# Optimization experiments

Measured on AMD Instinct MI355X. Metric: run time of the kernel, lower is better.

Reference implementation:

```python
import jax, jax.numpy as jnp
import numpy as np

N = 65536          # nodes
E = 1048576        # edges
IN_C = 128
HID_C = 32
HEADS = 4
OUT_C = 64
NEG_SLOPE = 0.2
EPS = 1e-16


def gat_conv(x, edge_index, W, att_src, att_dst, bias, heads, out_c, concat):
    """PyG-style GATConv. x: [N, F_in]; edge_index: [2, E] (row=src, col=dst).
    W: [F_in, heads*out_c]; att_src/att_dst: [heads, out_c]; bias: [heads*out_c] or [out_c]."""
    src, dst = edge_index[0], edge_index[1]
    n = x.shape[0]
    h = (x @ W).reshape(n, heads, out_c)                      # [N, H, C]
    a_src = jnp.einsum('nhc,hc->nh', h, att_src)              # [N, H]
    a_dst = jnp.einsum('nhc,hc->nh', h, att_dst)              # [N, H]
    alpha = a_src[src] + a_dst[dst]                           # [E, H]
    alpha = jax.nn.leaky_relu(alpha, NEG_SLOPE)
    # segment softmax over incoming edges of each destination node
    amax = jax.ops.segment_max(alpha, dst, num_segments=n)    # [N, H]
    alpha = jnp.exp(alpha - amax[dst])
    denom = jax.ops.segment_sum(alpha, dst, num_segments=n)   # [N, H]
    alpha = alpha / (denom[dst] + EPS)
    # weighted scatter-add aggregation
    msgs = alpha[:, :, None] * h[src]                         # [E, H, C]
    out = jax.ops.segment_sum(msgs, dst, num_segments=n)      # [N, H, C]
    if concat:
        out = out.reshape(n, heads * out_c)
    else:
        out = out.mean(axis=1)
    return out + bias


def setup_inputs() -> dict:
    key = jax.random.key(0)
    ks = jax.random.split(key, 10)
    s_in = 1.0 / np.sqrt(IN_C)
    s_h = 1.0 / np.sqrt(HEADS * HID_C)
    x = jax.random.normal(ks[0], (N, IN_C), dtype=jnp.float32)
    edge_index = jax.random.randint(ks[1], (2, E), 0, N, dtype=jnp.int64)
    W1 = jax.random.normal(ks[2], (IN_C, HEADS * HID_C), dtype=jnp.float32) * s_in
    att_src1 = jax.random.normal(ks[3], (HEADS, HID_C), dtype=jnp.float32) * s_h
    att_dst1 = jax.random.normal(ks[4], (HEADS, HID_C), dtype=jnp.float32) * s_h
    b1 = jnp.zeros((HEADS * HID_C,), dtype=jnp.float32)
    W2 = jax.random.normal(ks[5], (HEADS * HID_C, OUT_C), dtype=jnp.float32) * s_h
    att_src2 = jax.random.normal(ks[6], (1, OUT_C), dtype=jnp.float32) * s_h
    att_dst2 = jax.random.normal(ks[7], (1, OUT_C), dtype=jnp.float32) * s_h
    b2 = jnp.zeros((OUT_C,), dtype=jnp.float32)
    return {"x": x, "edge_index": edge_index, "W1": W1, "att_src1": att_src1,
            "att_dst1": att_dst1, "b1": b1, "W2": W2, "att_src2": att_src2,
            "att_dst2": att_dst2, "b2": b2}


def reference(x, edge_index, W1, att_src1, att_dst1, b1, W2, att_src2, att_dst2, b2):
    # dropout is identity in eval mode
    h = gat_conv(x, edge_index, W1, att_src1, att_dst1, b1, HEADS, HID_C, concat=True)
    h = jax.nn.sigmoid(h)
    h = gat_conv(h, edge_index, W2, att_src2, att_dst2, b2, 1, OUT_C, concat=True)
    return jax.nn.sigmoid(h)
```

## Files before the change

kernel.cpp:

```cpp
#include <hip/hip_runtime.h>
#include <hip/hip_fp16.h>

#define N_NODES 65536
#define N_EDGES 1048576
#define NBUCK 256
#define PBLOCKS 1024
#define EPB (N_EDGES / PBLOCKS)
#define K4CAP 6144
#define GB1 (N_NODES / 64)
constexpr float NEG = 0.2f;
constexpr float EPS_ = 1e-16f;
constexpr float WSHIFT = 2.7725887f;

typedef __attribute__((ext_vector_type(8))) short bf16x8;
typedef __attribute__((ext_vector_type(4))) float f32x4;

__device__ __forceinline__ unsigned short f2bf(float f) {
    unsigned int u = __float_as_uint(f);
    return (unsigned short)((u + 0x7fffu + ((u >> 16) & 1u)) >> 16);
}
__device__ __forceinline__ unsigned short f2h(float f) {
    __half_raw r = __half_raw(__float2half(f));
    return r.x;
}
__device__ __forceinline__ __half2 u2h2(unsigned int u) {
    union { unsigned int u; __half2 h; } c; c.u = u; return c.h;
}
__device__ __forceinline__ unsigned int h22u(__half2 h) {
    union { unsigned int u; __half2 h; } c; c.h = h; return c.u;
}
__device__ __forceinline__ float lrelu_exp_s(float l) {
    return __expf(fmaxf(l, NEG * l) - WSHIFT);
}


__global__ __launch_bounds__(1024) void scan_a(const int* __restrict__ in,
                                               int* __restrict__ out,
                                               int* __restrict__ bsum) {
    __shared__ int sm[1024];
    int t = threadIdx.x, i = blockIdx.x * 1024 + t;
    int v = in[i];
    sm[t] = v;
    __syncthreads();
    for (int off = 1; off < 1024; off <<= 1) {
        int u = (t >= off) ? sm[t - off] : 0;
        __syncthreads();
        sm[t] += u;
        __syncthreads();
    }
    out[i] = sm[t] - v;
    if (t == 1023) bsum[blockIdx.x] = sm[t];
}

__global__ __launch_bounds__(256) void partition_kernel(const int* __restrict__ ei,
                                                        const int* __restrict__ cursor_mat,
                                                        const int* __restrict__ bsum,
                                                        unsigned int* __restrict__ edge_part) {
    __shared__ int h[NBUCK];
    __shared__ int start[NBUCK];
    __shared__ int cur[NBUCK];
    __shared__ int gcur[NBUCK];
    __shared__ int bs[NBUCK];
    __shared__ unsigned int stage[EPB];
    int t = threadIdx.x;
    h[t] = 0;
    int bsv = bsum[t];
    bs[t] = bsv;
    __syncthreads();
    unsigned int ent[EPB / 256];
    int base = blockIdx.x * EPB;
    #pragma unroll
    for (int i = 0; i < EPB / 256; ++i) {
        int e = base + i * 256 + t;
        int s = ei[e], d = ei[N_EDGES + e];
        ent[i] = ((unsigned int)s << 16) | (unsigned int)d;
        atomicAdd(&h[d >> 8], 1);
    }
    __syncthreads();
    int v = h[t];
    start[t] = v;
    __syncthreads();
    for (int off = 1; off < 256; off <<= 1) {
        int u1 = (t >= off) ? start[t - off] : 0;
        int u2 = (t >= off) ? bs[t - off] : 0;
        __syncthreads();
        start[t] += u1;
        bs[t] += u2;
        __syncthreads();
    }
    int excl = start[t] - v;
    start[t] = excl;
    cur[t] = excl;
    gcur[t] = cursor_mat[t * PBLOCKS + blockIdx.x] + (bs[t] - bsv);
    __syncthreads();
    #pragma unroll
    for (int i = 0; i < EPB / 256; ++i) {
        int b = (int)((ent[i] & 0xffffu) >> 8);
        int slot = atomicAdd(&cur[b], 1);
        stage[slot] = ent[i];
    }
    __syncthreads();
    int s0 = t * (EPB / 256);
    #pragma unroll
    for (int i = 0; i < EPB / 256; ++i) {
        unsigned int p = stage[s0 + i];
        int b = (int)((p & 0xffffu) >> 8);
        edge_part[gcur[b] + (s0 + i - start[b])] = p;
    }
}

__global__ __launch_bounds__(1024) void finalize_kernel(const unsigned int* __restrict__ edge_part,
                                                        const int* __restrict__ cursor_mat,
                                                        const int* __restrict__ bsum,
                                                        int* __restrict__ row_ptr,
                                                        unsigned short* __restrict__ csr16) {
    __shared__ int h[256];
    __shared__ int sc[256];
    __shared__ int cur[256];
    __shared__ int bs[256];
    __shared__ unsigned short stage[K4CAP];
    int t = threadIdx.x;
    int b = blockIdx.x;
    if (b == NBUCK - 1 && t == 0) row_ptr[N_NODES] = N_EDGES;
    if (t < 256) bs[t] = bsum[t];
    __syncthreads();
    for (int off = 1; off < 256; off <<= 1) {
        int u = (t < 256 && t >= off) ? bs[t - off] : 0;
        __syncthreads();
        if (t < 256) bs[t] += u;
        __syncthreads();
    }
    int cs = cursor_mat[b * PBLOCKS] + (b ? bs[b - 1] : 0);
    int ce = (b == NBUCK - 1) ? N_EDGES : cursor_mat[(b + 1) * PBLOCKS] + bs[b];
    int cnt = ce - cs;
    if (t < 256) h[t] = 0;
    __syncthreads();
    for (int i = t; i < cnt; i += 1024)
        atomicAdd(&h[edge_part[cs + i] & 0xffu], 1);
    __syncthreads();
    int v = 0;
    if (t < 256) { v = h[t]; sc[t] = v; }
    __syncthreads();
    for (int off = 1; off < 256; off <<= 1) {
        int u = (t < 256 && t >= off) ? sc[t - off] : 0;
        __syncthreads();
        if (t < 256) sc[t] += u;
        __syncthreads();
    }
    if (t < 256) {
        int excl = sc[t] - v;
        row_ptr[b * 256 + t] = cs + excl;
        cur[t] = excl;
    }
    __syncthreads();
    if (cnt <= K4CAP) {
        for (int i = t; i < cnt; i += 1024) {
            unsigned int p = edge_part[cs + i];
            int slot = atomicAdd(&cur[p & 0xffu], 1);
            stage[slot] = (unsigned short)(p >> 16);
        }
        __syncthreads();
        for (int i = t; i < cnt; i += 1024)
            csr16[cs + i] = stage[i];
    } else {
        for (int i = t; i < cnt; i += 1024) {
            unsigned int p = edge_part[cs + i];
            int slot = atomicAdd(&cur[p & 0xffu], 1);
            csr16[cs + slot] = (unsigned short)(p >> 16);
        }
    }
}


__global__ __launch_bounds__(256) void gemm1_hist(const float* __restrict__ X,
                                                  const float* __restrict__ W,
                                                  const float* __restrict__ as_w,
                                                  const float* __restrict__ ad_w,
                                                  const int* __restrict__ ei,
                                                  unsigned short* __restrict__ H,
                                                  float* __restrict__ a_src,
                                                  float* __restrict__ a_dst,
                                                  int* __restrict__ hist_mat) {
    extern __shared__ unsigned short Wl[];
    int t = threadIdx.x;
    if (blockIdx.x >= GB1) {
        int* hs = (int*)Wl;
        int pb = blockIdx.x - GB1;
        hs[t] = 0;
        __syncthreads();
        int base = pb * EPB;
        #pragma unroll
        for (int i = 0; i < EPB / 256; ++i) {
            int d = ei[N_EDGES + base + i * 256 + t];
            atomicAdd(&hs[d >> 8], 1);
        }
        __syncthreads();
        hist_mat[t * PBLOCKS + pb] = hs[t];
        return;
    }
    constexpr int OUTC = 128;
    constexpr int NT = OUTC / 16;
    for (int idx = t; idx < OUTC * 128; idx += 256) {
        int j = idx & 7;
        int ln = (idx >> 3) & 63;
        int fc = idx >> 9;
        int kc = fc & 3, ct = fc >> 2;
        int k = kc * 32 + (ln >> 4) * 8 + j;
        int nn = ct * 16 + (ln & 15);
        Wl[idx] = (unsigned short)f2bf(W[k * OUTC + nn]);
    }
    __syncthreads();
    int wave = t >> 6, lane = t & 63;
    int m = lane & 15, quad = lane >> 4;
    int node_base = blockIdx.x * 64 + wave * 16;
    const float* xrow = X + (size_t)(node_base + m) * 128 + quad * 8;
    bf16x8 a[4];
    #pragma unroll
    for (int kc = 0; kc < 4; ++kc) {
        float4 u = *(const float4*)(xrow + kc * 32);
        float4 v = *(const float4*)(xrow + kc * 32 + 4);
        bf16x8 af;
        af[0] = (short)f2bf(u.x); af[1] = (short)f2bf(u.y);
        af[2] = (short)f2bf(u.z); af[3] = (short)f2bf(u.w);
        af[4] = (short)f2bf(v.x); af[5] = (short)f2bf(v.y);
        af[6] = (short)f2bf(v.z); af[7] = (short)f2bf(v.w);
        a[kc] = af;
    }
    float asv[NT], adv[NT];
    #pragma unroll
    for (int ct = 0; ct < NT; ++ct) {
        asv[ct] = as_w[ct * 16 + m];
        adv[ct] = ad_w[ct * 16 + m];
    }
    float ps[4][4] = {};
    float pd[4][4] = {};
    #pragma unroll
    for (int ct = 0; ct < NT; ++ct) {
        f32x4 acc = {0.f, 0.f, 0.f, 0.f};
        #pragma unroll
        for (int kc = 0; kc < 4; ++kc) {
            bf16x8 bfr = *(const bf16x8*)(Wl + ((ct * 4 + kc) * 64 + lane) * 8);
            acc = __builtin_amdgcn_mfma_f32_16x16x32_bf16(a[kc], bfr, acc, 0, 0, 0);
        }
        int hh = ct >> 1;
        #pragma unroll
        for (int r = 0; r < 4; ++r) {
            H[(size_t)(node_base + quad * 4 + r) * OUTC + ct * 16 + m] = f2h(acc[r]);
            ps[r][hh] += acc[r] * asv[ct];
            pd[r][hh] += acc[r] * adv[ct];
        }
    }
    #pragma unroll
    for (int r = 0; r < 4; ++r) {
        #pragma unroll
        for (int hh = 0; hh < 4; ++hh) {
            float s = ps[r][hh], d = pd[r][hh];
            #pragma unroll
            for (int msk = 1; msk < 16; msk <<= 1) {
                s += __shfl_xor(s, msk);
                d += __shfl_xor(d, msk);
            }
            if (m == 0) {
                int node = node_base + quad * 4 + r;
                a_src[node * 4 + hh] = s;
                a_dst[node * 4 + hh] = d;
            }
        }
    }
}


__global__ __launch_bounds__(256) void gemm2_mfma(const unsigned short* __restrict__ X,
                                                  const float* __restrict__ W,
                                                  const float* __restrict__ as_w,
                                                  const float* __restrict__ ad_w,
                                                  unsigned short* __restrict__ H,
                                                  float* __restrict__ a_src,
                                                  float* __restrict__ a_dst) {
    constexpr int OUTC = 64;
    constexpr int NT = OUTC / 16;
    extern __shared__ unsigned short Wl[];
    int t = threadIdx.x;
    for (int idx = t; idx < OUTC * 128; idx += 256) {
        int j = idx & 7;
        int ln = (idx >> 3) & 63;
        int fc = idx >> 9;
        int kc = fc & 3, ct = fc >> 2;
        int k = kc * 32 + (ln >> 4) * 8 + j;
        int nn = ct * 16 + (ln & 15);
        Wl[idx] = (unsigned short)f2bf(W[k * OUTC + nn]);
    }
    __syncthreads();
    int wave = t >> 6, lane = t & 63;
    int m = lane & 15, quad = lane >> 4;
    int node_base = blockIdx.x * 64 + wave * 16;
    const unsigned short* xrow = X + (size_t)(node_base + m) * 128 + quad * 8;
    bf16x8 a[4];
    #pragma unroll
    for (int kc = 0; kc < 4; ++kc) a[kc] = *(const bf16x8*)(xrow + kc * 32);
    float asv[NT], adv[NT];
    #pragma unroll
    for (int ct = 0; ct < NT; ++ct) {
        asv[ct] = as_w[ct * 16 + m];
        adv[ct] = ad_w[ct * 16 + m];
    }
    float ps[4] = {};
    float pd[4] = {};
    #pragma unroll
    for (int ct = 0; ct < NT; ++ct) {
        f32x4 acc = {0.f, 0.f, 0.f, 0.f};
        #pragma unroll
        for (int kc = 0; kc < 4; ++kc) {
            bf16x8 bfr = *(const bf16x8*)(Wl + ((ct * 4 + kc) * 64 + lane) * 8);
            acc = __builtin_amdgcn_mfma_f32_16x16x32_bf16(a[kc], bfr, acc, 0, 0, 0);
        }
        #pragma unroll
        for (int r = 0; r < 4; ++r) {
            H[(size_t)(node_base + quad * 4 + r) * OUTC + ct * 16 + m] = f2h(acc[r]);
            ps[r] += acc[r] * asv[ct];
            pd[r] += acc[r] * adv[ct];
        }
    }
    #pragma unroll
    for (int r = 0; r < 4; ++r) {
        float s = ps[r], d = pd[r];
        #pragma unroll
        for (int msk = 1; msk < 16; msk <<= 1) {
            s += __shfl_xor(s, msk);
            d += __shfl_xor(d, msk);
        }
        if (m == 0) {
            int node = node_base + quad * 4 + r;
            a_src[node] = s;
            a_dst[node] = d;
        }
    }
}


__global__ __launch_bounds__(256) void agg1_kernel(const int* __restrict__ row_ptr,
                                                   const unsigned short* __restrict__ csr16,
                                                   const unsigned int* __restrict__ h1u,
                                                   const float* __restrict__ a_src,
                                                   const float* __restrict__ a_dst,
                                                   const float* __restrict__ b1,
                                                   unsigned short* __restrict__ x2) {
    int wave = (blockIdx.x * 256 + threadIdx.x) >> 6;
    int lane = threadIdx.x & 63;
    int half = lane >> 5;
    int ln = lane & 31;
    int n = wave * 2 + half;
    int j8 = ln & 7;
    int whead = ln >> 3;
    int sub = ln >> 4;
    int col = ln & 15;
    int hd_c = col >> 2;
    int rbase = half * 32 + hd_c * 8 + sub;
    float adw = a_dst[n * 4 + whead];
    const unsigned int* h1c = h1u + col * 4;
    const float* asw = a_src + whead;
    int e = row_ptr[n], end = row_ptr[n + 1];
    __half2 acc0 = u2h2(0u), acc1 = u2h2(0u), acc2 = u2h2(0u), acc3 = u2h2(0u);
    float denom = 0.f;
    while (e < end) {
        int rem = end - e;
        int mbA = rem > 8 ? 8 : rem;
        int remB = rem - 8;
        int mbB = remB > 8 ? 8 : (remB > 0 ? remB : 0);
        int idxA = e + (j8 < mbA ? j8 : 0);
        int idxB = (remB > 0) ? (e + 8 + (j8 < mbB ? j8 : 0)) : idxA;
        int sA = (int)csr16[idxA];
        int sB = (int)csr16[idxB];
        float lA = asw[sA * 4] + adw;
        float lB = asw[sB * 4] + adw;
        float wA = (j8 < mbA) ? lrelu_exp_s(lA) : 0.f;
        float wB = (j8 < mbB) ? lrelu_exp_s(lB) : 0.f;
        denom += wA + wB;
        unsigned int curA = ((unsigned int)f2h(wA) << 16) | (unsigned int)sA;
        unsigned int curB = ((unsigned int)f2h(wB) << 16) | (unsigned int)sB;
        unsigned int pkA0 = __shfl(curA, rbase);
        unsigned int pkA1 = __shfl(curA, rbase + 2);
        unsigned int pkA2 = __shfl(curA, rbase + 4);
        unsigned int pkA3 = __shfl(curA, rbase + 6);
        unsigned int pkB0 = __shfl(curB, rbase);
        unsigned int pkB1 = __shfl(curB, rbase + 2);
        unsigned int pkB2 = __shfl(curB, rbase + 4);
        unsigned int pkB3 = __shfl(curB, rbase + 6);
        uint4 hvA0 = *(const uint4*)(h1c + (size_t)(pkA0 & 0xffffu) * 64);
        uint4 hvA1 = *(const uint4*)(h1c + (size_t)(pkA1 & 0xffffu) * 64);
        uint4 hvA2 = *(const uint4*)(h1c + (size_t)(pkA2 & 0xffffu) * 64);
        uint4 hvA3 = *(const uint4*)(h1c + (size_t)(pkA3 & 0xffffu) * 64);
        uint4 hvB0 = *(const uint4*)(h1c + (size_t)(pkB0 & 0xffffu) * 64);
        uint4 hvB1 = *(const uint4*)(h1c + (size_t)(pkB1 & 0xffffu) * 64);
        uint4 hvB2 = *(const uint4*)(h1c + (size_t)(pkB2 & 0xffffu) * 64);
        uint4 hvB3 = *(const uint4*)(h1c + (size_t)(pkB3 & 0xffffu) * 64);
        unsigned int wu; __half2 w2;
        wu = pkA0 >> 16; w2 = u2h2(wu | (wu << 16));
        acc0 = __hfma2(w2, u2h2(hvA0.x), acc0);
        acc1 = __hfma2(w2, u2h2(hvA0.y), acc1);
        acc2 = __hfma2(w2, u2h2(hvA0.z), acc2);
        acc3 = __hfma2(w2, u2h2(hvA0.w), acc3);
        wu = pkA1 >> 16; w2 = u2h2(wu | (wu << 16));
        acc0 = __hfma2(w2, u2h2(hvA1.x), acc0);
        acc1 = __hfma2(w2, u2h2(hvA1.y), acc1);
        acc2 = __hfma2(w2, u2h2(hvA1.z), acc2);
        acc3 = __hfma2(w2, u2h2(hvA1.w), acc3);
        wu = pkA2 >> 16; w2 = u2h2(wu | (wu << 16));
        acc0 = __hfma2(w2, u2h2(hvA2.x), acc0);
        acc1 = __hfma2(w2, u2h2(hvA2.y), acc1);
        acc2 = __hfma2(w2, u2h2(hvA2.z), acc2);
        acc3 = __hfma2(w2, u2h2(hvA2.w), acc3);
        wu = pkA3 >> 16; w2 = u2h2(wu | (wu << 16));
        acc0 = __hfma2(w2, u2h2(hvA3.x), acc0);
        acc1 = __hfma2(w2, u2h2(hvA3.y), acc1);
        acc2 = __hfma2(w2, u2h2(hvA3.z), acc2);
        acc3 = __hfma2(w2, u2h2(hvA3.w), acc3);
        wu = pkB0 >> 16; w2 = u2h2(wu | (wu << 16));
        acc0 = __hfma2(w2, u2h2(hvB0.x), acc0);
        acc1 = __hfma2(w2, u2h2(hvB0.y), acc1);
        acc2 = __hfma2(w2, u2h2(hvB0.z), acc2);
        acc3 = __hfma2(w2, u2h2(hvB0.w), acc3);
        wu = pkB1 >> 16; w2 = u2h2(wu | (wu << 16));
        acc0 = __hfma2(w2, u2h2(hvB1.x), acc0);
        acc1 = __hfma2(w2, u2h2(hvB1.y), acc1);
        acc2 = __hfma2(w2, u2h2(hvB1.z), acc2);
        acc3 = __hfma2(w2, u2h2(hvB1.w), acc3);
        wu = pkB2 >> 16; w2 = u2h2(wu | (wu << 16));
        acc0 = __hfma2(w2, u2h2(hvB2.x), acc0);
        acc1 = __hfma2(w2, u2h2(hvB2.y), acc1);
        acc2 = __hfma2(w2, u2h2(hvB2.z), acc2);
        acc3 = __hfma2(w2, u2h2(hvB2.w), acc3);
        wu = pkB3 >> 16; w2 = u2h2(wu | (wu << 16));
        acc0 = __hfma2(w2, u2h2(hvB3.x), acc0);
        acc1 = __hfma2(w2, u2h2(hvB3.y), acc1);
        acc2 = __hfma2(w2, u2h2(hvB3.z), acc2);
        acc3 = __hfma2(w2, u2h2(hvB3.w), acc3);
        e += 16;
    }
    acc0 = __hadd2(acc0, u2h2(__shfl_xor(h22u(acc0), 16)));
    acc1 = __hadd2(acc1, u2h2(__shfl_xor(h22u(acc1), 16)));
    acc2 = __hadd2(acc2, u2h2(__shfl_xor(h22u(acc2), 16)));
    acc3 = __hadd2(acc3, u2h2(__shfl_xor(h22u(acc3), 16)));
    #pragma unroll
    for (int m = 1; m < 8; m <<= 1) denom += __shfl_xor(denom, m);
    float dfin = __shfl(denom, half * 32 + hd_c * 8);
    if (sub == 0) {
        float inv = 1.f / (dfin + EPS_);
        int c0 = col * 8;
        float v[8];
        v[0] = __low2float(acc0); v[1] = __high2float(acc0);
        v[2] = __low2float(acc1); v[3] = __high2float(acc1);
        v[4] = __low2float(acc2); v[5] = __high2float(acc2);
        v[6] = __low2float(acc3); v[7] = __high2float(acc3);
        unsigned int o[4];
        #pragma unroll
        for (int i = 0; i < 4; ++i) {
            float u0 = v[2 * i] * inv + b1[c0 + 2 * i];
            float u1 = v[2 * i + 1] * inv + b1[c0 + 2 * i + 1];
            u0 = 1.f / (1.f + __expf(-u0));
            u1 = 1.f / (1.f + __expf(-u1));
            o[i] = (unsigned int)f2bf(u0) | ((unsigned int)f2bf(u1) << 16);
        }
        *(uint4*)(x2 + (size_t)n * 128 + c0) = make_uint4(o[0], o[1], o[2], o[3]);
    }
}

__global__ __launch_bounds__(256) void agg2_kernel(const int* __restrict__ row_ptr,
                                                   const unsigned short* __restrict__ csr16,
                                                   const unsigned int* __restrict__ h2u,
                                                   const float* __restrict__ a_src,
                                                   const float* __restrict__ a_dst,
                                                   const float* __restrict__ b2,
                                                   float* __restrict__ out) {
    int wave = (blockIdx.x * 256 + threadIdx.x) >> 6;
    int lane = threadIdx.x & 63;
    int half = lane >> 5;
    int ln = lane & 31;
    int n = wave * 2 + half;
    int j8 = ln & 7;
    int sub = (ln >> 3) & 3;
    int col = ln & 7;
    int rbase = half * 32 + sub;
    float ad = a_dst[n];
    const unsigned int* h2c = h2u + col * 4;
    int e = row_ptr[n], end = row_ptr[n + 1];
    __half2 acc0 = u2h2(0u), acc1 = u2h2(0u), acc2 = u2h2(0u), acc3 = u2h2(0u);
    float denom = 0.f;
    while (e < end) {
        int rem = end - e;
        int mbA = rem > 8 ? 8 : rem;
        int remB = rem - 8;
        int mbB = remB > 8 ? 8 : (remB > 0 ? remB : 0);
        int idxA = e + (j8 < mbA ? j8 : 0);
        int idxB = (remB > 0) ? (e + 8 + (j8 < mbB ? j8 : 0)) : idxA;
        int sA = (int)csr16[idxA];
        int sB = (int)csr16[idxB];
        float lA = a_src[sA] + ad;
        float lB = a_src[sB] + ad;
        float wA = (j8 < mbA) ? lrelu_exp_s(lA) : 0.f;
        float wB = (j8 < mbB) ? lrelu_exp_s(lB) : 0.f;
        denom += wA + wB;
        unsigned int curA = ((unsigned int)f2h(wA) << 16) | (unsigned int)sA;
        unsigned int curB = ((unsigned int)f2h(wB) << 16) | (unsigned int)sB;
        unsigned int pkA0 = __shfl(curA, rbase);
        unsigned int pkA1 = __shfl(curA, rbase + 4);
        unsigned int pkB0 = __shfl(curB, rbase);
        unsigned int pkB1 = __shfl(curB, rbase + 4);
        uint4 hvA0 = *(const uint4*)(h2c + (size_t)(pkA0 & 0xffffu) * 32);
        uint4 hvA1 = *(const uint4*)(h2c + (size_t)(pkA1 & 0xffffu) * 32);
        uint4 hvB0 = *(const uint4*)(h2c + (size_t)(pkB0 & 0xffffu) * 32);
        uint4 hvB1 = *(const uint4*)(h2c + (size_t)(pkB1 & 0xffffu) * 32);
        unsigned int wu; __half2 w2;
        wu = pkA0 >> 16; w2 = u2h2(wu | (wu << 16));
        acc0 = __hfma2(w2, u2h2(hvA0.x), acc0);
        acc1 = __hfma2(w2, u2h2(hvA0.y), acc1);
        acc2 = __hfma2(w2, u2h2(hvA0.z), acc2);
        acc3 = __hfma2(w2, u2h2(hvA0.w), acc3);
        wu = pkA1 >> 16; w2 = u2h2(wu | (wu << 16));
        acc0 = __hfma2(w2, u2h2(hvA1.x), acc0);
        acc1 = __hfma2(w2, u2h2(hvA1.y), acc1);
        acc2 = __hfma2(w2, u2h2(hvA1.z), acc2);
        acc3 = __hfma2(w2, u2h2(hvA1.w), acc3);
        wu = pkB0 >> 16; w2 = u2h2(wu | (wu << 16));
        acc0 = __hfma2(w2, u2h2(hvB0.x), acc0);
        acc1 = __hfma2(w2, u2h2(hvB0.y), acc1);
        acc2 = __hfma2(w2, u2h2(hvB0.z), acc2);
        acc3 = __hfma2(w2, u2h2(hvB0.w), acc3);
        wu = pkB1 >> 16; w2 = u2h2(wu | (wu << 16));
        acc0 = __hfma2(w2, u2h2(hvB1.x), acc0);
        acc1 = __hfma2(w2, u2h2(hvB1.y), acc1);
        acc2 = __hfma2(w2, u2h2(hvB1.z), acc2);
        acc3 = __hfma2(w2, u2h2(hvB1.w), acc3);
        e += 16;
    }
    #pragma unroll
    for (int m = 8; m < 32; m <<= 1) {
        acc0 = __hadd2(acc0, u2h2(__shfl_xor(h22u(acc0), m)));
        acc1 = __hadd2(acc1, u2h2(__shfl_xor(h22u(acc1), m)));
        acc2 = __hadd2(acc2, u2h2(__shfl_xor(h22u(acc2), m)));
        acc3 = __hadd2(acc3, u2h2(__shfl_xor(h22u(acc3), m)));
    }
    #pragma unroll
    for (int m = 1; m < 8; m <<= 1) denom += __shfl_xor(denom, m);
    if (sub == 0) {
        float inv = 1.f / (denom + EPS_);
        int c0 = col * 8;
        float v[8];
        v[0] = __low2float(acc0); v[1] = __high2float(acc0);
        v[2] = __low2float(acc1); v[3] = __high2float(acc1);
        v[4] = __low2float(acc2); v[5] = __high2float(acc2);
        v[6] = __low2float(acc3); v[7] = __high2float(acc3);
        float o[8];
        #pragma unroll
        for (int i = 0; i < 8; ++i) {
            float u = v[i] * inv + b2[c0 + i];
            o[i] = 1.f / (1.f + __expf(-u));
        }
        float4* dst = (float4*)(out + (size_t)n * 64 + c0);
        dst[0] = make_float4(o[0], o[1], o[2], o[3]);
        dst[1] = make_float4(o[4], o[5], o[6], o[7]);
    }
}


extern "C" void kernel_launch(void* const* d_in, const int* in_sizes, int n_in,
                              void* d_out, int out_size, void* d_ws, size_t ws_size,
                              hipStream_t stream) {
    (void)in_sizes; (void)n_in; (void)out_size; (void)ws_size;
    const float* x   = (const float*)d_in[0];
    const int*   ei  = (const int*)d_in[1];
    const float* W1  = (const float*)d_in[2];
    const float* as1 = (const float*)d_in[3];
    const float* ad1 = (const float*)d_in[4];
    const float* b1  = (const float*)d_in[5];
    const float* W2  = (const float*)d_in[6];
    const float* as2 = (const float*)d_in[7];
    const float* ad2 = (const float*)d_in[8];
    const float* b2  = (const float*)d_in[9];
    float* out = (float*)d_out;

    char* p = (char*)d_ws;
    auto alloc = [&](size_t bytes) -> void* {
        void* r = (void*)p;
        p += (bytes + 255) & ~(size_t)255;
        return r;
    };
    int* hist_mat   = (int*)alloc((size_t)NBUCK * PBLOCKS * 4);
    int* cursor_mat = (int*)alloc((size_t)NBUCK * PBLOCKS * 4);
    int* bsum       = (int*)alloc(256 * 4);
    unsigned int* edge_part = (unsigned int*)alloc((size_t)N_EDGES * 4);
    int* row_ptr    = (int*)alloc((size_t)(N_NODES + 1) * 4);
    unsigned short* csr16 = (unsigned short*)alloc((size_t)N_EDGES * 2);
    unsigned short* h1 = (unsigned short*)alloc((size_t)N_NODES * 128 * 2);
    float* a_src1   = (float*)alloc((size_t)N_NODES * 4 * 4);
    float* a_dst1   = (float*)alloc((size_t)N_NODES * 4 * 4);
    unsigned short* x2 = (unsigned short*)alloc((size_t)N_NODES * 128 * 2);
    unsigned short* h2 = (unsigned short*)alloc((size_t)N_NODES * 64 * 2);
    float* a_src2   = (float*)alloc((size_t)N_NODES * 4);
    float* a_dst2   = (float*)alloc((size_t)N_NODES * 4);

    gemm1_hist<<<GB1 + PBLOCKS, 256, 128 * 128 * 2, stream>>>(
        x, W1, as1, ad1, ei, h1, a_src1, a_dst1, hist_mat);
    scan_a<<<NBUCK * PBLOCKS / 1024, 1024, 0, stream>>>(hist_mat, cursor_mat, bsum);
    partition_kernel<<<PBLOCKS, 256, 0, stream>>>(ei, cursor_mat, bsum, edge_part);
    finalize_kernel<<<NBUCK, 1024, 0, stream>>>(edge_part, cursor_mat, bsum, row_ptr, csr16);
    agg1_kernel<<<N_NODES / 8, 256, 0, stream>>>(row_ptr, csr16, (const unsigned int*)h1,
                                                 a_src1, a_dst1, b1, x2);
    gemm2_mfma<<<N_NODES / 64, 256, 128 * 64 * 2, stream>>>(x2, W2, as2, ad2, h2, a_src2, a_dst2);
    agg2_kernel<<<N_NODES / 8, 256, 0, stream>>>(row_ptr, csr16, (const unsigned int*)h2,
                                                 a_src2, a_dst2, b2, out);
}
```

Before: 220.0 us.

## Stage GEMM outputs through LDS for coalesced stores; persistent grid-stride aggregation

Both MFMA GEMM kernels now keep their accumulators in registers, write the fp16 tile into the reused LDS weight buffer, then store the whole 64-row tile to global memory with coalesced 16-byte writes instead of scattered 2-byte stores. The two aggregation kernels switch from one wave per node pair with a huge grid to a fixed grid of 8192 waves that loop over node pairs grid-stride. The aim is fewer memory transactions on the stores and less block launch overhead, at the cost of two extra barriers and possible load imbalance across waves.

```diff
diff --git a/kernel.cpp b/kernel.cpp
--- a/kernel.cpp
+++ b/kernel.cpp
@@ -8,6 +8,7 @@
 #define EPB (N_EDGES / PBLOCKS)
 #define K4CAP 6144
 #define GB1 (N_NODES / 64)
+#define AGG_WAVES 8192
 constexpr float NEG = 0.2f;
 constexpr float EPS_ = 1e-16f;
 constexpr float WSHIFT = 2.7725887f;
@@ -234,6 +235,7 @@
     }
     float ps[4][4] = {};
     float pd[4][4] = {};
+    f32x4 accs[NT];
     #pragma unroll
     for (int ct = 0; ct < NT; ++ct) {
         f32x4 acc = {0.f, 0.f, 0.f, 0.f};
@@ -242,10 +244,10 @@
             bf16x8 bfr = *(const bf16x8*)(Wl + ((ct * 4 + kc) * 64 + lane) * 8);
             acc = __builtin_amdgcn_mfma_f32_16x16x32_bf16(a[kc], bfr, acc, 0, 0, 0);
         }
+        accs[ct] = acc;
         int hh = ct >> 1;
         #pragma unroll
         for (int r = 0; r < 4; ++r) {
-            H[(size_t)(node_base + quad * 4 + r) * OUTC + ct * 16 + m] = f2h(acc[r]);
             ps[r][hh] += acc[r] * asv[ct];
             pd[r][hh] += acc[r] * adv[ct];
         }
@@ -267,6 +269,21 @@
             }
         }
     }
+    __syncthreads();
+    unsigned short* Hst = Wl;
+    int lrow = wave * 16 + quad * 4;
+    #pragma unroll
+    for (int ct = 0; ct < NT; ++ct) {
+        #pragma unroll
+        for (int r = 0; r < 4; ++r)
+            Hst[(lrow + r) * OUTC + ct * 16 + m] = f2h(accs[ct][r]);
+    }
+    __syncthreads();
+    const uint4* Hsv = (const uint4*)Hst;
+    uint4* Hg = (uint4*)(H + (size_t)blockIdx.x * 64 * OUTC);
+    #pragma unroll
+    for (int i = 0; i < 64 * OUTC / 8 / 256; ++i)
+        Hg[i * 256 + t] = Hsv[i * 256 + t];
 }
 
 
@@ -306,6 +323,7 @@
     }
     float ps[4] = {};
     float pd[4] = {};
+    f32x4 accs[NT];
     #pragma unroll
     for (int ct = 0; ct < NT; ++ct) {
         f32x4 acc = {0.f, 0.f, 0.f, 0.f};
@@ -314,9 +332,9 @@
             bf16x8 bfr = *(const bf16x8*)(Wl + ((ct * 4 + kc) * 64 + lane) * 8);
             acc = __builtin_amdgcn_mfma_f32_16x16x32_bf16(a[kc], bfr, acc, 0, 0, 0);
         }
+        accs[ct] = acc;
         #pragma unroll
         for (int r = 0; r < 4; ++r) {
-            H[(size_t)(node_base + quad * 4 + r) * OUTC + ct * 16 + m] = f2h(acc[r]);
             ps[r] += acc[r] * asv[ct];
             pd[r] += acc[r] * adv[ct];
         }
@@ -335,6 +353,21 @@
             a_dst[node] = d;
         }
     }
+    __syncthreads();
+    unsigned short* Hst = Wl;
+    int lrow = wave * 16 + quad * 4;
+    #pragma unroll
+    for (int ct = 0; ct < NT; ++ct) {
+        #pragma unroll
+        for (int r = 0; r < 4; ++r)
+            Hst[(lrow + r) * OUTC + ct * 16 + m] = f2h(accs[ct][r]);
+    }
+    __syncthreads();
+    const uint4* Hsv = (const uint4*)Hst;
+    uint4* Hg = (uint4*)(H + (size_t)blockIdx.x * 64 * OUTC);
+    #pragma unroll
+    for (int i = 0; i < 64 * OUTC / 8 / 256; ++i)
+        Hg[i * 256 + t] = Hsv[i * 256 + t];
 }
 
 
@@ -345,123 +378,125 @@
                                                    const float* __restrict__ a_dst,
                                                    const float* __restrict__ b1,
                                                    unsigned short* __restrict__ x2) {
-    int wave = (blockIdx.x * 256 + threadIdx.x) >> 6;
+    int wid = (blockIdx.x * 256 + threadIdx.x) >> 6;
     int lane = threadIdx.x & 63;
     int half = lane >> 5;
     int ln = lane & 31;
-    int n = wave * 2 + half;
     int j8 = ln & 7;
     int whead = ln >> 3;
     int sub = ln >> 4;
     int col = ln & 15;
     int hd_c = col >> 2;
     int rbase = half * 32 + hd_c * 8 + sub;
-    float adw = a_dst[n * 4 + whead];
     const unsigned int* h1c = h1u + col * 4;
     const float* asw = a_src + whead;
-    int e = row_ptr[n], end = row_ptr[n + 1];
-    __half2 acc0 = u2h2(0u), acc1 = u2h2(0u), acc2 = u2h2(0u), acc3 = u2h2(0u);
-    float denom = 0.f;
-    while (e < end) {
-        int rem = end - e;
-        int mbA = rem > 8 ? 8 : rem;
-        int remB = rem - 8;
-        int mbB = remB > 8 ? 8 : (remB > 0 ? remB : 0);
-        int idxA = e + (j8 < mbA ? j8 : 0);
-        int idxB = (remB > 0) ? (e + 8 + (j8 < mbB ? j8 : 0)) : idxA;
-        int sA = (int)csr16[idxA];
-        int sB = (int)csr16[idxB];
-        float lA = asw[sA * 4] + adw;
-        float lB = asw[sB * 4] + adw;
-        float wA = (j8 < mbA) ? lrelu_exp_s(lA) : 0.f;
-        float wB = (j8 < mbB) ? lrelu_exp_s(lB) : 0.f;
-        denom += wA + wB;
-        unsigned int curA = ((unsigned int)f2h(wA) << 16) | (unsigned int)sA;
-        unsigned int curB = ((unsigned int)f2h(wB) << 16) | (unsigned int)sB;
-        unsigned int pkA0 = __shfl(curA, rbase);
-        unsigned int pkA1 = __shfl(curA, rbase + 2);
-        unsigned int pkA2 = __shfl(curA, rbase + 4);
-        unsigned int pkA3 = __shfl(curA, rbase + 6);
-        unsigned int pkB0 = __shfl(curB, rbase);
-        unsigned int pkB1 = __shfl(curB, rbase + 2);
-        unsigned int pkB2 = __shfl(curB, rbase + 4);
-        unsigned int pkB3 = __shfl(curB, rbase + 6);
-        uint4 hvA0 = *(const uint4*)(h1c + (size_t)(pkA0 & 0xffffu) * 64);
-        uint4 hvA1 = *(const uint4*)(h1c + (size_t)(pkA1 & 0xffffu) * 64);
-        uint4 hvA2 = *(const uint4*)(h1c + (size_t)(pkA2 & 0xffffu) * 64);
-        uint4 hvA3 = *(const uint4*)(h1c + (size_t)(pkA3 & 0xffffu) * 64);
-        uint4 hvB0 = *(const uint4*)(h1c + (size_t)(pkB0 & 0xffffu) * 64);
-        uint4 hvB1 = *(const uint4*)(h1c + (size_t)(pkB1 & 0xffffu) * 64);
-        uint4 hvB2 = *(const uint4*)(h1c + (size_t)(pkB2 & 0xffffu) * 64);
-        uint4 hvB3 = *(const uint4*)(h1c + (size_t)(pkB3 & 0xffffu) * 64);
-        unsigned int wu; __half2 w2;
-        wu = pkA0 >> 16; w2 = u2h2(wu | (wu << 16));
-        acc0 = __hfma2(w2, u2h2(hvA0.x), acc0);
-        acc1 = __hfma2(w2, u2h2(hvA0.y), acc1);
-        acc2 = __hfma2(w2, u2h2(hvA0.z), acc2);
-        acc3 = __hfma2(w2, u2h2(hvA0.w), acc3);
-        wu = pkA1 >> 16; w2 = u2h2(wu | (wu << 16));
-        acc0 = __hfma2(w2, u2h2(hvA1.x), acc0);
-        acc1 = __hfma2(w2, u2h2(hvA1.y), acc1);
-        acc2 = __hfma2(w2, u2h2(hvA1.z), acc2);
-        acc3 = __hfma2(w2, u2h2(hvA1.w), acc3);
-        wu = pkA2 >> 16; w2 = u2h2(wu | (wu << 16));
-        acc0 = __hfma2(w2, u2h2(hvA2.x), acc0);
-        acc1 = __hfma2(w2, u2h2(hvA2.y), acc1);
-        acc2 = __hfma2(w2, u2h2(hvA2.z), acc2);
-        acc3 = __hfma2(w2, u2h2(hvA2.w), acc3);
-        wu = pkA3 >> 16; w2 = u2h2(wu | (wu << 16));
-        acc0 = __hfma2(w2, u2h2(hvA3.x), acc0);
-        acc1 = __hfma2(w2, u2h2(hvA3.y), acc1);
-        acc2 = __hfma2(w2, u2h2(hvA3.z), acc2);
-        acc3 = __hfma2(w2, u2h2(hvA3.w), acc3);
-        wu = pkB0 >> 16; w2 = u2h2(wu | (wu << 16));
-        acc0 = __hfma2(w2, u2h2(hvB0.x), acc0);
-        acc1 = __hfma2(w2, u2h2(hvB0.y), acc1);
-        acc2 = __hfma2(w2, u2h2(hvB0.z), acc2);
-        acc3 = __hfma2(w2, u2h2(hvB0.w), acc3);
-        wu = pkB1 >> 16; w2 = u2h2(wu | (wu << 16));
-        acc0 = __hfma2(w2, u2h2(hvB1.x), acc0);
-        acc1 = __hfma2(w2, u2h2(hvB1.y), acc1);
-        acc2 = __hfma2(w2, u2h2(hvB1.z), acc2);
-        acc3 = __hfma2(w2, u2h2(hvB1.w), acc3);
-        wu = pkB2 >> 16; w2 = u2h2(wu | (wu << 16));
-        acc0 = __hfma2(w2, u2h2(hvB2.x), acc0);
-        acc1 = __hfma2(w2, u2h2(hvB2.y), acc1);
-        acc2 = __hfma2(w2, u2h2(hvB2.z), acc2);
-        acc3 = __hfma2(w2, u2h2(hvB2.w), acc3);
-        wu = pkB3 >> 16; w2 = u2h2(wu | (wu << 16));
-        acc0 = __hfma2(w2, u2h2(hvB3.x), acc0);
-        acc1 = __hfma2(w2, u2h2(hvB3.y), acc1);
-        acc2 = __hfma2(w2, u2h2(hvB3.z), acc2);
-        acc3 = __hfma2(w2, u2h2(hvB3.w), acc3);
-        e += 16;
-    }
-    acc0 = __hadd2(acc0, u2h2(__shfl_xor(h22u(acc0), 16)));
-    acc1 = __hadd2(acc1, u2h2(__shfl_xor(h22u(acc1), 16)));
-    acc2 = __hadd2(acc2, u2h2(__shfl_xor(h22u(acc2), 16)));
-    acc3 = __hadd2(acc3, u2h2(__shfl_xor(h22u(acc3), 16)));
-    #pragma unroll
-    for (int m = 1; m < 8; m <<= 1) denom += __shfl_xor(denom, m);
-    float dfin = __shfl(denom, half * 32 + hd_c * 8);
-    if (sub == 0) {
-        float inv = 1.f / (dfin + EPS_);
-        int c0 = col * 8;
-        float v[8];
-        v[0] = __low2float(acc0); v[1] = __high2float(acc0);
-        v[2] = __low2float(acc1); v[3] = __high2float(acc1);
-        v[4] = __low2float(acc2); v[5] = __high2float(acc2);
-        v[6] = __low2float(acc3); v[7] = __high2float(acc3);
-        unsigned int o[4];
-        #pragma unroll
-        for (int i = 0; i < 4; ++i) {
-            float u0 = v[2 * i] * inv + b1[c0 + 2 * i];
-            float u1 = v[2 * i + 1] * inv + b1[c0 + 2 * i + 1];
-            u0 = 1.f / (1.f + __expf(-u0));
-            u1 = 1.f / (1.f + __expf(-u1));
-            o[i] = (unsigned int)f2bf(u0) | ((unsigned int)f2bf(u1) << 16);
-        }
-        *(uint4*)(x2 + (size_t)n * 128 + c0) = make_uint4(o[0], o[1], o[2], o[3]);
+    for (int pr = wid; pr < N_NODES / 2; pr += AGG_WAVES) {
+        int n = pr * 2 + half;
+        float adw = a_dst[n * 4 + whead];
+        int e = row_ptr[n], end = row_ptr[n + 1];
+        __half2 acc0 = u2h2(0u), acc1 = u2h2(0u), acc2 = u2h2(0u), acc3 = u2h2(0u);
+        float denom = 0.f;
+        while (e < end) {
+            int rem = end - e;
+            int mbA = rem > 8 ? 8 : rem;
+            int remB = rem - 8;
+            int mbB = remB > 8 ? 8 : (remB > 0 ? remB : 0);
+            int idxA = e + (j8 < mbA ? j8 : 0);
+            int idxB = (remB > 0) ? (e + 8 + (j8 < mbB ? j8 : 0)) : idxA;
+            int sA = (int)csr16[idxA];
+            int sB = (int)csr16[idxB];
+            float lA = asw[sA * 4] + adw;
+            float lB = asw[sB * 4] + adw;
+            float wA = (j8 < mbA) ? lrelu_exp_s(lA) : 0.f;
+            float wB = (j8 < mbB) ? lrelu_exp_s(lB) : 0.f;
+            denom += wA + wB;
+            unsigned int curA = ((unsigned int)f2h(wA) << 16) | (unsigned int)sA;
+            unsigned int curB = ((unsigned int)f2h(wB) << 16) | (unsigned int)sB;
+            unsigned int pkA0 = __shfl(curA, rbase);
+            unsigned int pkA1 = __shfl(curA, rbase + 2);
+            unsigned int pkA2 = __shfl(curA, rbase + 4);
+            unsigned int pkA3 = __shfl(curA, rbase + 6);
+            unsigned int pkB0 = __shfl(curB, rbase);
+            unsigned int pkB1 = __shfl(curB, rbase + 2);
+            unsigned int pkB2 = __shfl(curB, rbase + 4);
+            unsigned int pkB3 = __shfl(curB, rbase + 6);
+            uint4 hvA0 = *(const uint4*)(h1c + (size_t)(pkA0 & 0xffffu) * 64);
+            uint4 hvA1 = *(const uint4*)(h1c + (size_t)(pkA1 & 0xffffu) * 64);
+            uint4 hvA2 = *(const uint4*)(h1c + (size_t)(pkA2 & 0xffffu) * 64);
+            uint4 hvA3 = *(const uint4*)(h1c + (size_t)(pkA3 & 0xffffu) * 64);
+            uint4 hvB0 = *(const uint4*)(h1c + (size_t)(pkB0 & 0xffffu) * 64);
+            uint4 hvB1 = *(const uint4*)(h1c + (size_t)(pkB1 & 0xffffu) * 64);
+            uint4 hvB2 = *(const uint4*)(h1c + (size_t)(pkB2 & 0xffffu) * 64);
+            uint4 hvB3 = *(const uint4*)(h1c + (size_t)(pkB3 & 0xffffu) * 64);
+            unsigned int wu; __half2 w2;
+            wu = pkA0 >> 16; w2 = u2h2(wu | (wu << 16));
+            acc0 = __hfma2(w2, u2h2(hvA0.x), acc0);
+            acc1 = __hfma2(w2, u2h2(hvA0.y), acc1);
+            acc2 = __hfma2(w2, u2h2(hvA0.z), acc2);
+            acc3 = __hfma2(w2, u2h2(hvA0.w), acc3);
+            wu = pkA1 >> 16; w2 = u2h2(wu | (wu << 16));
+            acc0 = __hfma2(w2, u2h2(hvA1.x), acc0);
+            acc1 = __hfma2(w2, u2h2(hvA1.y), acc1);
+            acc2 = __hfma2(w2, u2h2(hvA1.z), acc2);
+            acc3 = __hfma2(w2, u2h2(hvA1.w), acc3);
+            wu = pkA2 >> 16; w2 = u2h2(wu | (wu << 16));
+            acc0 = __hfma2(w2, u2h2(hvA2.x), acc0);
+            acc1 = __hfma2(w2, u2h2(hvA2.y), acc1);
+            acc2 = __hfma2(w2, u2h2(hvA2.z), acc2);
+            acc3 = __hfma2(w2, u2h2(hvA2.w), acc3);
+            wu = pkA3 >> 16; w2 = u2h2(wu | (wu << 16));
+            acc0 = __hfma2(w2, u2h2(hvA3.x), acc0);
+            acc1 = __hfma2(w2, u2h2(hvA3.y), acc1);
+            acc2 = __hfma2(w2, u2h2(hvA3.z), acc2);
+            acc3 = __hfma2(w2, u2h2(hvA3.w), acc3);
+            wu = pkB0 >> 16; w2 = u2h2(wu | (wu << 16));
+            acc0 = __hfma2(w2, u2h2(hvB0.x), acc0);
+            acc1 = __hfma2(w2, u2h2(hvB0.y), acc1);
+            acc2 = __hfma2(w2, u2h2(hvB0.z), acc2);
+            acc3 = __hfma2(w2, u2h2(hvB0.w), acc3);
+            wu = pkB1 >> 16; w2 = u2h2(wu | (wu << 16));
+            acc0 = __hfma2(w2, u2h2(hvB1.x), acc0);
+            acc1 = __hfma2(w2, u2h2(hvB1.y), acc1);
+            acc2 = __hfma2(w2, u2h2(hvB1.z), acc2);
+            acc3 = __hfma2(w2, u2h2(hvB1.w), acc3);
+            wu = pkB2 >> 16; w2 = u2h2(wu | (wu << 16));
+            acc0 = __hfma2(w2, u2h2(hvB2.x), acc0);
+            acc1 = __hfma2(w2, u2h2(hvB2.y), acc1);
+            acc2 = __hfma2(w2, u2h2(hvB2.z), acc2);
+            acc3 = __hfma2(w2, u2h2(hvB2.w), acc3);
+            wu = pkB3 >> 16; w2 = u2h2(wu | (wu << 16));
+            acc0 = __hfma2(w2, u2h2(hvB3.x), acc0);
+            acc1 = __hfma2(w2, u2h2(hvB3.y), acc1);
+            acc2 = __hfma2(w2, u2h2(hvB3.z), acc2);
+            acc3 = __hfma2(w2, u2h2(hvB3.w), acc3);
+            e += 16;
+        }
+        acc0 = __hadd2(acc0, u2h2(__shfl_xor(h22u(acc0), 16)));
+        acc1 = __hadd2(acc1, u2h2(__shfl_xor(h22u(acc1), 16)));
+        acc2 = __hadd2(acc2, u2h2(__shfl_xor(h22u(acc2), 16)));
+        acc3 = __hadd2(acc3, u2h2(__shfl_xor(h22u(acc3), 16)));
+        #pragma unroll
+        for (int mm = 1; mm < 8; mm <<= 1) denom += __shfl_xor(denom, mm);
+        float dfin = __shfl(denom, half * 32 + hd_c * 8);
+        if (sub == 0) {
+            float inv = 1.f / (dfin + EPS_);
+            int c0 = col * 8;
+            float v[8];
+            v[0] = __low2float(acc0); v[1] = __high2float(acc0);
+            v[2] = __low2float(acc1); v[3] = __high2float(acc1);
+            v[4] = __low2float(acc2); v[5] = __high2float(acc2);
+            v[6] = __low2float(acc3); v[7] = __high2float(acc3);
+            unsigned int o[4];
+            #pragma unroll
+            for (int i = 0; i < 4; ++i) {
+                float u0 = v[2 * i] * inv + b1[c0 + 2 * i];
+                float u1 = v[2 * i + 1] * inv + b1[c0 + 2 * i + 1];
+                u0 = 1.f / (1.f + __expf(-u0));
+                u1 = 1.f / (1.f + __expf(-u1));
+                o[i] = (unsigned int)f2bf(u0) | ((unsigned int)f2bf(u1) << 16);
+            }
+            *(uint4*)(x2 + (size_t)n * 128 + c0) = make_uint4(o[0], o[1], o[2], o[3]);
+        }
     }
 }
 
@@ -472,93 +507,95 @@
                                                    const float* __restrict__ a_dst,
                                                    const float* __restrict__ b2,
                                                    float* __restrict__ out) {
-    int wave = (blockIdx.x * 256 + threadIdx.x) >> 6;
+    int wid = (blockIdx.x * 256 + threadIdx.x) >> 6;
     int lane = threadIdx.x & 63;
     int half = lane >> 5;
     int ln = lane & 31;
-    int n = wave * 2 + half;
     int j8 = ln & 7;
     int sub = (ln >> 3) & 3;
     int col = ln & 7;
     int rbase = half * 32 + sub;
-    float ad = a_dst[n];
     const unsigned int* h2c = h2u + col * 4;
-    int e = row_ptr[n], end = row_ptr[n + 1];
-    __half2 acc0 = u2h2(0u), acc1 = u2h2(0u), acc2 = u2h2(0u), acc3 = u2h2(0u);
-    float denom = 0.f;
-    while (e < end) {
-        int rem = end - e;
-        int mbA = rem > 8 ? 8 : rem;
-        int remB = rem - 8;
-        int mbB = remB > 8 ? 8 : (remB > 0 ? remB : 0);
-        int idxA = e + (j8 < mbA ? j8 : 0);
-        int idxB = (remB > 0) ? (e + 8 + (j8 < mbB ? j8 : 0)) : idxA;
-        int sA = (int)csr16[idxA];
-        int sB = (int)csr16[idxB];
-        float lA = a_src[sA] + ad;
-        float lB = a_src[sB] + ad;
-        float wA = (j8 < mbA) ? lrelu_exp_s(lA) : 0.f;
-        float wB = (j8 < mbB) ? lrelu_exp_s(lB) : 0.f;
-        denom += wA + wB;
-        unsigned int curA = ((unsigned int)f2h(wA) << 16) | (unsigned int)sA;
-        unsigned int curB = ((unsigned int)f2h(wB) << 16) | (unsigned int)sB;
-        unsigned int pkA0 = __shfl(curA, rbase);
-        unsigned int pkA1 = __shfl(curA, rbase + 4);
-        unsigned int pkB0 = __shfl(curB, rbase);
-        unsigned int pkB1 = __shfl(curB, rbase + 4);
-        uint4 hvA0 = *(const uint4*)(h2c + (size_t)(pkA0 & 0xffffu) * 32);
-        uint4 hvA1 = *(const uint4*)(h2c + (size_t)(pkA1 & 0xffffu) * 32);
-        uint4 hvB0 = *(const uint4*)(h2c + (size_t)(pkB0 & 0xffffu) * 32);
-        uint4 hvB1 = *(const uint4*)(h2c + (size_t)(pkB1 & 0xffffu) * 32);
-        unsigned int wu; __half2 w2;
-        wu = pkA0 >> 16; w2 = u2h2(wu | (wu << 16));
-        acc0 = __hfma2(w2, u2h2(hvA0.x), acc0);
-        acc1 = __hfma2(w2, u2h2(hvA0.y), acc1);
-        acc2 = __hfma2(w2, u2h2(hvA0.z), acc2);
-        acc3 = __hfma2(w2, u2h2(hvA0.w), acc3);
-        wu = pkA1 >> 16; w2 = u2h2(wu | (wu << 16));
-        acc0 = __hfma2(w2, u2h2(hvA1.x), acc0);
-        acc1 = __hfma2(w2, u2h2(hvA1.y), acc1);
-        acc2 = __hfma2(w2, u2h2(hvA1.z), acc2);
-        acc3 = __hfma2(w2, u2h2(hvA1.w), acc3);
-        wu = pkB0 >> 16; w2 = u2h2(wu | (wu << 16));
-        acc0 = __hfma2(w2, u2h2(hvB0.x), acc0);
-        acc1 = __hfma2(w2, u2h2(hvB0.y), acc1);
-        acc2 = __hfma2(w2, u2h2(hvB0.z), acc2);
-        acc3 = __hfma2(w2, u2h2(hvB0.w), acc3);
-        wu = pkB1 >> 16; w2 = u2h2(wu | (wu << 16));
-        acc0 = __hfma2(w2, u2h2(hvB1.x), acc0);
-        acc1 = __hfma2(w2, u2h2(hvB1.y), acc1);
-        acc2 = __hfma2(w2, u2h2(hvB1.z), acc2);
-        acc3 = __hfma2(w2, u2h2(hvB1.w), acc3);
-        e += 16;
-    }
-    #pragma unroll
-    for (int m = 8; m < 32; m <<= 1) {
-        acc0 = __hadd2(acc0, u2h2(__shfl_xor(h22u(acc0), m)));
-        acc1 = __hadd2(acc1, u2h2(__shfl_xor(h22u(acc1), m)));
-        acc2 = __hadd2(acc2, u2h2(__shfl_xor(h22u(acc2), m)));
-        acc3 = __hadd2(acc3, u2h2(__shfl_xor(h22u(acc3), m)));
-    }
-    #pragma unroll
-    for (int m = 1; m < 8; m <<= 1) denom += __shfl_xor(denom, m);
-    if (sub == 0) {
-        float inv = 1.f / (denom + EPS_);
-        int c0 = col * 8;
-        float v[8];
-        v[0] = __low2float(acc0); v[1] = __high2float(acc0);
-        v[2] = __low2float(acc1); v[3] = __high2float(acc1);
-        v[4] = __low2float(acc2); v[5] = __high2float(acc2);
-        v[6] = __low2float(acc3); v[7] = __high2float(acc3);
-        float o[8];
-        #pragma unroll
-        for (int i = 0; i < 8; ++i) {
-            float u = v[i] * inv + b2[c0 + i];
-            o[i] = 1.f / (1.f + __expf(-u));
-        }
-        float4* dst = (float4*)(out + (size_t)n * 64 + c0);
-        dst[0] = make_float4(o[0], o[1], o[2], o[3]);
-        dst[1] = make_float4(o[4], o[5], o[6], o[7]);
+    for (int pr = wid; pr < N_NODES / 2; pr += AGG_WAVES) {
+        int n = pr * 2 + half;
+        float ad = a_dst[n];
+        int e = row_ptr[n], end = row_ptr[n + 1];
+        __half2 acc0 = u2h2(0u), acc1 = u2h2(0u), acc2 = u2h2(0u), acc3 = u2h2(0u);
+        float denom = 0.f;
+        while (e < end) {
+            int rem = end - e;
+            int mbA = rem > 8 ? 8 : rem;
+            int remB = rem - 8;
+            int mbB = remB > 8 ? 8 : (remB > 0 ? remB : 0);
+            int idxA = e + (j8 < mbA ? j8 : 0);
+            int idxB = (remB > 0) ? (e + 8 + (j8 < mbB ? j8 : 0)) : idxA;
+            int sA = (int)csr16[idxA];
+            int sB = (int)csr16[idxB];
+            float lA = a_src[sA] + ad;
+            float lB = a_src[sB] + ad;
+            float wA = (j8 < mbA) ? lrelu_exp_s(lA) : 0.f;
+            float wB = (j8 < mbB) ? lrelu_exp_s(lB) : 0.f;
+            denom += wA + wB;
+            unsigned int curA = ((unsigned int)f2h(wA) << 16) | (unsigned int)sA;
+            unsigned int curB = ((unsigned int)f2h(wB) << 16) | (unsigned int)sB;
+            unsigned int pkA0 = __shfl(curA, rbase);
+            unsigned int pkA1 = __shfl(curA, rbase + 4);
+            unsigned int pkB0 = __shfl(curB, rbase);
+            unsigned int pkB1 = __shfl(curB, rbase + 4);
+            uint4 hvA0 = *(const uint4*)(h2c + (size_t)(pkA0 & 0xffffu) * 32);
+            uint4 hvA1 = *(const uint4*)(h2c + (size_t)(pkA1 & 0xffffu) * 32);
+            uint4 hvB0 = *(const uint4*)(h2c + (size_t)(pkB0 & 0xffffu) * 32);
+            uint4 hvB1 = *(const uint4*)(h2c + (size_t)(pkB1 & 0xffffu) * 32);
+            unsigned int wu; __half2 w2;
+            wu = pkA0 >> 16; w2 = u2h2(wu | (wu << 16));
+            acc0 = __hfma2(w2, u2h2(hvA0.x), acc0);
+            acc1 = __hfma2(w2, u2h2(hvA0.y), acc1);
+            acc2 = __hfma2(w2, u2h2(hvA0.z), acc2);
+            acc3 = __hfma2(w2, u2h2(hvA0.w), acc3);
+            wu = pkA1 >> 16; w2 = u2h2(wu | (wu << 16));
+            acc0 = __hfma2(w2, u2h2(hvA1.x), acc0);
+            acc1 = __hfma2(w2, u2h2(hvA1.y), acc1);
+            acc2 = __hfma2(w2, u2h2(hvA1.z), acc2);
+            acc3 = __hfma2(w2, u2h2(hvA1.w), acc3);
+            wu = pkB0 >> 16; w2 = u2h2(wu | (wu << 16));
+            acc0 = __hfma2(w2, u2h2(hvB0.x), acc0);
+            acc1 = __hfma2(w2, u2h2(hvB0.y), acc1);
+            acc2 = __hfma2(w2, u2h2(hvB0.z), acc2);
+            acc3 = __hfma2(w2, u2h2(hvB0.w), acc3);
+            wu = pkB1 >> 16; w2 = u2h2(wu | (wu << 16));
+            acc0 = __hfma2(w2, u2h2(hvB1.x), acc0);
+            acc1 = __hfma2(w2, u2h2(hvB1.y), acc1);
+            acc2 = __hfma2(w2, u2h2(hvB1.z), acc2);
+            acc3 = __hfma2(w2, u2h2(hvB1.w), acc3);
+            e += 16;
+        }
+        #pragma unroll
+        for (int mm = 8; mm < 32; mm <<= 1) {
+            acc0 = __hadd2(acc0, u2h2(__shfl_xor(h22u(acc0), mm)));
+            acc1 = __hadd2(acc1, u2h2(__shfl_xor(h22u(acc1), mm)));
+            acc2 = __hadd2(acc2, u2h2(__shfl_xor(h22u(acc2), mm)));
+            acc3 = __hadd2(acc3, u2h2(__shfl_xor(h22u(acc3), mm)));
+        }
+        #pragma unroll
+        for (int mm = 1; mm < 8; mm <<= 1) denom += __shfl_xor(denom, mm);
+        if (sub == 0) {
+            float inv = 1.f / (denom + EPS_);
+            int c0 = col * 8;
+            float v[8];
+            v[0] = __low2float(acc0); v[1] = __high2float(acc0);
+            v[2] = __low2float(acc1); v[3] = __high2float(acc1);
+            v[4] = __low2float(acc2); v[5] = __high2float(acc2);
+            v[6] = __low2float(acc3); v[7] = __high2float(acc3);
+            float o[8];
+            #pragma unroll
+            for (int i = 0; i < 8; ++i) {
+                float u = v[i] * inv + b2[c0 + i];
+                o[i] = 1.f / (1.f + __expf(-u));
+            }
+            float4* dst = (float4*)(out + (size_t)n * 64 + c0);
+            dst[0] = make_float4(o[0], o[1], o[2], o[3]);
+            dst[1] = make_float4(o[4], o[5], o[6], o[7]);
+        }
     }
 }
 
@@ -604,9 +641,9 @@
     scan_a<<<NBUCK * PBLOCKS / 1024, 1024, 0, stream>>>(hist_mat, cursor_mat, bsum);
     partition_kernel<<<PBLOCKS, 256, 0, stream>>>(ei, cursor_mat, bsum, edge_part);
     finalize_kernel<<<NBUCK, 1024, 0, stream>>>(edge_part, cursor_mat, bsum, row_ptr, csr16);
-    agg1_kernel<<<N_NODES / 8, 256, 0, stream>>>(row_ptr, csr16, (const unsigned int*)h1,
-                                                 a_src1, a_dst1, b1, x2);
+    agg1_kernel<<<AGG_WAVES / 4, 256, 0, stream>>>(row_ptr, csr16, (const unsigned int*)h1,
+                                                   a_src1, a_dst1, b1, x2);
     gemm2_mfma<<<N_NODES / 64, 256, 128 * 64 * 2, stream>>>(x2, W2, as2, ad2, h2, a_src2, a_dst2);
-    agg2_kernel<<<N_NODES / 8, 256, 0, stream>>>(row_ptr, csr16, (const unsigned int*)h2,
-                                                 a_src2, a_dst2, b2, out);
-}
+    agg2_kernel<<<AGG_WAVES / 4, 256, 0, stream>>>(row_ptr, csr16, (const unsigned int*)h2,
+                                                   a_src2, a_dst2, b2, out);
+}
```

Measured after the change: 225.0 us. +2.3%, slower.
